# Performance work log

Hardware: AMD Instinct MI355X
Metric: run time of the kernel (lower is better)

Reference implementation:

```python
import jax, jax.numpy as jnp
import numpy as np

L = 28          # num_hidden_layers (kv_cache leading dim = 2*L = 56)
H = 1024        # hidden_size
NH = 8          # num_attention_heads
KVH = 4         # num_key_value_heads
HD = 128        # head_dim
I = 3072        # mlp intermediate size
VC = 4096       # codec vocab size
NCG = 16        # num_code_groups
B = 4
S = 512         # cached seq len
THETA = 1000000.0
EPS = 1e-6


def rmsnorm(x, w):
    v = jnp.mean(jnp.square(x.astype(jnp.float32)), axis=-1, keepdims=True)
    return (x * jax.lax.rsqrt(v + EPS)).astype(x.dtype) * w


def rotate_half(x):
    h = x.shape[-1] // 2
    return jnp.concatenate([-x[..., h:], x[..., :h]], axis=-1)


def setup_inputs() -> dict:
    key = jax.random.key(0)
    ks = jax.random.split(key, 16)
    def f(k, shp, s=0.02):
        return jax.random.normal(k, shp, jnp.float32) * s
    return {
        "cb0_id": jax.random.randint(ks[0], (B, 1), 0, VC),
        "cb1_15_ids": jax.random.randint(ks[1], (B, NCG - 1), 0, VC),
        "trailing_text_embed": f(ks[2], (B, 1, H), 1.0),
        "kv_cache": f(ks[3], (2 * L, B, KVH, S, HD), 1.0),
        "position": jnp.full((B,), S, dtype=jnp.int32),
        "cb0_emb": f(ks[4], (VC, H), 1.0),
        "cp_emb": f(ks[5], (NCG - 1, VC, H), 1.0),
        "Wq": f(ks[6], (L, H, NH * HD)),
        "Wk": f(ks[7], (L, H, KVH * HD)),
        "Wv": f(ks[8], (L, H, KVH * HD)),
        "Wo": f(ks[9], (L, NH * HD, H)),
        "q_norm_w": jnp.ones((L, HD), jnp.float32),
        "k_norm_w": jnp.ones((L, HD), jnp.float32),
        "ln1_w": jnp.ones((L, H), jnp.float32),
        "ln2_w": jnp.ones((L, H), jnp.float32),
        "Wgate": f(ks[10], (L, H, I)),
        "Wup": f(ks[11], (L, H, I)),
        "Wdown": f(ks[12], (L, I, H)),
        "norm_w": jnp.ones((H,), jnp.float32),
        "head_w": f(ks[13], (H, VC)),
    }


def reference(cb0_id, cb1_15_ids, trailing_text_embed, kv_cache, position,
              cb0_emb, cp_emb, Wq, Wk, Wv, Wo, q_norm_w, k_norm_w,
              ln1_w, ln2_w, Wgate, Wup, Wdown, norm_w, head_w):
    n_rep = NH // KVH
    scale = 1.0 / np.sqrt(HD).astype(np.float32)

    # --- codebook embedding sum ---
    e = cb0_emb[cb0_id[:, 0]]                                   # [B,H]
    cp = cp_emb[jnp.arange(NCG - 1)[None, :], cb1_15_ids]       # [B,15,H]
    h = (e + cp.sum(axis=1))[:, None, :] + trailing_text_embed  # [B,1,H]

    # --- rotary at current position; broadcast shape [B,1,1,HD] ---
    inv_freq = 1.0 / (THETA ** (jnp.arange(0, HD, 2, dtype=jnp.float32) / HD))
    freqs = position.astype(jnp.float32)[:, None] * inv_freq[None, :]  # [B,HD/2]
    emb = jnp.concatenate([freqs, freqs], axis=-1)              # [B,HD]
    cos = jnp.cos(emb)[:, None, None, :]
    sin = jnp.sin(emb)[:, None, None, :]

    kv = kv_cache.reshape(L, 2, B, KVH, S, HD)

    def layer(hs, xs):
        wq, wk, wv, wo, qn, kn, l1, l2, wg, wu, wd, kc, vc = xs
        x = rmsnorm(hs, l1)
        q = (x @ wq).reshape(B, 1, NH, HD)
        k = (x @ wk).reshape(B, 1, KVH, HD)
        v = (x @ wv).reshape(B, 1, KVH, HD)
        q = jnp.transpose(rmsnorm(q, qn), (0, 2, 1, 3))   # [B,NH,1,HD]
        k = jnp.transpose(rmsnorm(k, kn), (0, 2, 1, 3))   # [B,KVH,1,HD]
        v = jnp.transpose(v, (0, 2, 1, 3))
        q = q * cos + rotate_half(q) * sin
        k = k * cos + rotate_half(k) * sin
        fk = jnp.concatenate([kc, k], axis=2)             # [B,KVH,S+1,HD]
        fv = jnp.concatenate([vc, v], axis=2)
        # GQA: head h attends kv head h // n_rep == reshape grouping (q_len = 1)
        qg = q.reshape(B, KVH, n_rep, HD)
        scores = jnp.einsum('bgrd,bgsd->bgrs', qg, fk) * scale
        w = jax.nn.softmax(scores.astype(jnp.float32), axis=-1).astype(q.dtype)
        o = jnp.einsum('bgrs,bgsd->bgrd', w, fv).reshape(B, 1, NH * HD)
        hs = hs + o @ wo
        x = rmsnorm(hs, l2)
        hs = hs + (jax.nn.silu(x @ wg) * (x @ wu)) @ wd
        return hs, (k, v)

    xs = (Wq, Wk, Wv, Wo, q_norm_w, k_norm_w, ln1_w, ln2_w,
          Wgate, Wup, Wdown, kv[:, 0], kv[:, 1])
    h, (new_k, new_v) = jax.lax.scan(layer, h, xs)

    h = rmsnorm(h, norm_w)
    past_hidden = h                                       # [B,1,H]
    logits = (h @ head_w)[:, 0, :]                        # [B,VC]

    full_k = jnp.concatenate([kv[:, 0], new_k], axis=3)   # [L,B,KVH,S+1,HD]
    full_v = jnp.concatenate([kv[:, 1], new_v], axis=3)
    new_kv_cache = jnp.stack([full_k, full_v], axis=1).reshape(2 * L, B, KVH, S + 1, HD)
    return logits, new_kv_cache, past_hidden
```

## Files before the change

kernel.cpp:

```cpp
#include <hip/hip_runtime.h>
#include <math.h>

#define L_  28
#define H_  1024
#define NH_ 8
#define KVH_ 4
#define HD_ 128
#define I_  3072
#define VC_ 4096
#define B_  4
#define S_  512
#define EPS_ 1e-6f

#define WS_HA   0
#define WS_HB   4096
#define WS_X1   8192
#define WS_X2   12288
#define WS_XF   16384
#define WS_QKVP 20480
#define WS_ATTO 282624
#define WS_ATML 348160
#define WS_OPP  349184
#define WS_GUP  480256
#define WS_DWP  1266688
#define WS_HDP  1463296

__device__ __forceinline__ float wave_reduce_sum(float v) {
    #pragma unroll
    for (int off = 32; off; off >>= 1) v += __shfl_down(v, off);
    return v;
}
__device__ __forceinline__ float wave_reduce_max(float v) {
    #pragma unroll
    for (int off = 32; off; off >>= 1) v = fmaxf(v, __shfl_down(v, off));
    return v;
}

__global__ __launch_bounds__(256) void k_embed(
    const int* __restrict__ cb0, const int* __restrict__ cb1,
    const float* __restrict__ trail, const float* __restrict__ cb0e,
    const float* __restrict__ cpe, float* __restrict__ hA)
{
    int idx = blockIdx.x * 256 + threadIdx.x;
    int b = idx >> 10, i = idx & 1023;
    float v = cb0e[(size_t)cb0[b] * 1024 + i] + trail[idx];
    #pragma unroll
    for (int j = 0; j < 15; j++)
        v += cpe[((size_t)j * 4096 + cb1[b * 15 + j]) * 1024 + i];
    hA[idx] = v;
}

template<int P>
__global__ __launch_bounds__(1024) void k_norm(
    const float* __restrict__ base, const float* __restrict__ part,
    const float* __restrict__ w, float* __restrict__ hnew,
    float* __restrict__ xout, float* __restrict__ xout2)
{
    __shared__ float red[16];
    const int b = blockIdx.x, k = threadIdx.x;
    float v = base[b * 1024 + k];
    #pragma unroll
    for (int c = 0; c < P; c++) v += part[((size_t)c * 4 + b) * 1024 + k];
    hnew[b * 1024 + k] = v;
    float ss = wave_reduce_sum(v * v);
    if ((k & 63) == 0) red[k >> 6] = ss;
    __syncthreads();
    float tot = 0.f;
    #pragma unroll
    for (int i = 0; i < 16; i++) tot += red[i];
    const float rms = rsqrtf(tot * (1.f / 1024.f) + EPS_);
    const float x = v * rms * w[k];
    xout[b * 1024 + k] = x;
    if (xout2) xout2[b * 1024 + k] = x;
}

template<int RPC, int NTOT>
__device__ __forceinline__ void gemv_tail(
    const float* __restrict__ W, int ldw, int wcol0, int k0,
    const float* __restrict__ xsl, float4* __restrict__ accbuf,
    float* __restrict__ pp, int colblk, int ks)
{
    const int t = threadIdx.x;
    const int wv = t >> 6, lane = t & 63;
    constexpr int RPW = RPC / 4;
    const float4* xs4 = (const float4*)xsl;
    float4 a0 = {0,0,0,0}, a1 = {0,0,0,0}, a2 = {0,0,0,0}, a3 = {0,0,0,0};
    const float* Wp = W + (size_t)(k0 + wv * RPW) * ldw + wcol0 + lane * 4;
    #pragma unroll 8
    for (int i = 0; i < RPW; i++) {
        float4 wvv = *(const float4*)(Wp + (size_t)i * ldw);
        float4 xb = xs4[wv * RPW + i];
        a0.x += wvv.x * xb.x; a0.y += wvv.y * xb.x; a0.z += wvv.z * xb.x; a0.w += wvv.w * xb.x;
        a1.x += wvv.x * xb.y; a1.y += wvv.y * xb.y; a1.z += wvv.z * xb.y; a1.w += wvv.w * xb.y;
        a2.x += wvv.x * xb.z; a2.y += wvv.y * xb.z; a2.z += wvv.z * xb.z; a2.w += wvv.w * xb.z;
        a3.x += wvv.x * xb.w; a3.y += wvv.y * xb.w; a3.z += wvv.z * xb.w; a3.w += wvv.w * xb.w;
    }
    accbuf[(wv * 64 + lane) * 4 + 0] = a0;
    accbuf[(wv * 64 + lane) * 4 + 1] = a1;
    accbuf[(wv * 64 + lane) * 4 + 2] = a2;
    accbuf[(wv * 64 + lane) * 4 + 3] = a3;
    __syncthreads();
    const int l2 = t >> 2, b2 = t & 3;
    float4 s0 = accbuf[(0 * 64 + l2) * 4 + b2];
    float4 s1 = accbuf[(1 * 64 + l2) * 4 + b2];
    float4 s2 = accbuf[(2 * 64 + l2) * 4 + b2];
    float4 s3 = accbuf[(3 * 64 + l2) * 4 + b2];
    float4 s;
    s.x = s0.x + s1.x + s2.x + s3.x;
    s.y = s0.y + s1.y + s2.y + s3.y;
    s.z = s0.z + s1.z + s2.z + s3.z;
    s.w = s0.w + s1.w + s2.w + s3.w;
    *(float4*)(pp + ((size_t)ks * 4 + b2) * NTOT + colblk * 256 + l2 * 4) = s;
}

__global__ __launch_bounds__(256) void k_qkv(
    const float* __restrict__ x1,
    const float* __restrict__ Wq, const float* __restrict__ Wk,
    const float* __restrict__ Wv, float* __restrict__ qkvp)
{
    __shared__ float xsl[128];
    __shared__ float4 accbuf[1024];
    const int t = threadIdx.x;
    const int ks = blockIdx.y, k0 = ks * 32, cb = blockIdx.x;
    if (t < 128) { int kk = t & 31, b = t >> 5; xsl[kk * 4 + b] = x1[b * 1024 + k0 + kk]; }
    __syncthreads();
    const float* W; int ldw, wcol0;
    if (cb < 4)      { W = Wq; ldw = 1024; wcol0 = cb * 256; }
    else if (cb < 6) { W = Wk; ldw = 512;  wcol0 = (cb - 4) * 256; }
    else             { W = Wv; ldw = 512;  wcol0 = (cb - 6) * 256; }
    gemv_tail<32, 2048>(W, ldw, wcol0, k0, xsl, accbuf, qkvp, cb, ks);
}

__global__ __launch_bounds__(256) void k_attn(
    const float* __restrict__ qkvp,
    const float* __restrict__ qnw, const float* __restrict__ knw,
    const float* __restrict__ kin, const float* __restrict__ vin,
    float* __restrict__ kout, float* __restrict__ vout,
    const int* __restrict__ pos,
    float* __restrict__ opart, float* __restrict__ mlpart)
{
    __shared__ float Kl[33][129];
    __shared__ float Vl[33][129];
    __shared__ float ql[2][128];
    __shared__ float sc[2][36];
    __shared__ float red[8];

    const int t = threadIdx.x;
    const int bg = blockIdx.x, b = bg >> 2, g = bg & 3;
    const int c = blockIdx.y;
    const int lane = t & 63;
    const int r = t >> 7, d = t & 127;
    const float scale = 0.088388347648318447f;

    const float posf = (float)pos[b];
    const int j = d & 63;
    const float invf = powf(1.0e6f, -(float)j * (1.0f / 64.0f));
    const float ang = posf * invf;
    const float cs = cosf(ang), sn = sinf(ang);
    const int pd = (d < 64) ? d + 64 : d - 64;

    float qraw = 0.f;
    {
        const int n = (2 * g + r) * 128 + d;
        #pragma unroll
        for (int cc = 0; cc < 32; cc++) qraw += qkvp[((size_t)cc * 4 + b) * 2048 + n];
    }
    ql[r][d] = qraw;
    float ssq = wave_reduce_sum(qraw * qraw);
    if (lane == 0) red[t >> 6] = ssq;
    __syncthreads();
    const float rms_q = rsqrtf((red[r * 2] + red[r * 2 + 1]) * (1.f / 128.f) + EPS_);
    float qv = qraw * rms_q * qnw[d];
    float qp = ql[r][pd] * rms_q * qnw[pd];
    float qro = qv * cs + ((d < 64) ? -qp : qp) * sn;

    float kvraw = 0.f;
    if (c == 15) {
        const int base = (t < 128) ? (1024 + g * 128 + d) : (1536 + g * 128 + d);
        #pragma unroll
        for (int cc = 0; cc < 32; cc++) kvraw += qkvp[((size_t)cc * 4 + b) * 2048 + base];
    }
    float kss = wave_reduce_sum((t < 128) ? kvraw * kvraw : 0.f);
    __syncthreads();
    ql[r][d] = qro;
    if (lane == 0 && t < 128) red[t >> 6] = kss;
    if (c == 15) { if (t < 128) Kl[32][d] = kvraw; else Vl[32][d] = kvraw; }
    __syncthreads();
    float newkv = 0.f;
    if (c == 15) {
        if (t < 128) {
            const float rms_k = rsqrtf((red[0] + red[1]) * (1.f / 128.f) + EPS_);
            float kv_ = Kl[32][d] * rms_k * knw[d];
            float kp  = Kl[32][pd] * rms_k * knw[pd];
            newkv = kv_ * cs + ((d < 64) ? -kp : kp) * sn;
        } else {
            newkv = Vl[32][d];
        }
    }
    __syncthreads();
    const size_t out_bg = (size_t)bg * (513 * 128);
    if (c == 15) {
        if (t < 128) { Kl[32][d] = newkv; kout[out_bg + 512 * 128 + d] = newkv; }
        else         { Vl[32][d] = newkv; vout[out_bg + 512 * 128 + d] = newkv; }
    }

    const size_t in_bg = (size_t)bg * (512 * 128);
    const int s0 = c * 32;
    #pragma unroll
    for (int i = 0; i < 4; i++) {
        int f4 = i * 256 + t;
        int row = f4 >> 5, d0 = (f4 & 31) * 4;
        float4 k4 = *(const float4*)(kin + in_bg + (size_t)(s0 + row) * 128 + d0);
        float4 v4 = *(const float4*)(vin + in_bg + (size_t)(s0 + row) * 128 + d0);
        Kl[row][d0] = k4.x; Kl[row][d0 + 1] = k4.y; Kl[row][d0 + 2] = k4.z; Kl[row][d0 + 3] = k4.w;
        Vl[row][d0] = v4.x; Vl[row][d0 + 1] = v4.y; Vl[row][d0 + 2] = v4.z; Vl[row][d0 + 3] = v4.w;
        *(float4*)(kout + out_bg + (size_t)(s0 + row) * 128 + d0) = k4;
        *(float4*)(vout + out_bg + (size_t)(s0 + row) * 128 + d0) = v4;
    }
    __syncthreads();

    const int nk = (c == 15) ? 33 : 32;
    const int si = d;
    float sv = -1e30f;
    if (si < nk) {
        float a = 0.f;
        #pragma unroll 8
        for (int dd = 0; dd < 128; dd++) a += ql[r][dd] * Kl[si][dd];
        sv = a * scale;
    }
    float mv = wave_reduce_max(sv);
    if (lane == 0) red[t >> 6] = mv;
    __syncthreads();
    const float m = fmaxf(red[r * 2], red[r * 2 + 1]);
    float p = (si < nk) ? expf(sv - m) : 0.f;
    if (si < nk) sc[r][si] = p;
    float lsum = wave_reduce_sum(p);
    __syncthreads();
    if (lane == 0) red[t >> 6] = lsum;
    __syncthreads();
    const float lr = red[r * 2] + red[r * 2 + 1];
    if (d == 0) {
        mlpart[(size_t)((bg * 2 + r) * 16 + c) * 2 + 0] = m;
        mlpart[(size_t)((bg * 2 + r) * 16 + c) * 2 + 1] = lr;
    }
    float o = 0.f;
    for (int s2 = 0; s2 < nk; s2++) o += sc[r][s2] * Vl[s2][d];
    opart[(size_t)((bg * 2 + r) * 16 + c) * 128 + d] = o;
}

__global__ __launch_bounds__(256) void k_oproj(
    const float* __restrict__ atto, const float* __restrict__ atml,
    const float* __restrict__ Wo_l, float* __restrict__ opp)
{
    __shared__ float xsl[128];
    __shared__ float4 accbuf[1024];
    const int t = threadIdx.x;
    const int ks = blockIdx.y, k0 = ks * 32;
    if (t < 128) {
        const int kk = t & 31, b = t >> 5;
        const int nrow = k0 + kk;
        const int head = nrow >> 7, dh = nrow & 127;
        const int g = head >> 1, rr = head & 1;
        const size_t base = (size_t)((b * 4 + g) * 2 + rr) * 16;
        float mc[16], lc[16], M = -1e30f;
        #pragma unroll
        for (int cc = 0; cc < 16; cc++) {
            mc[cc] = atml[(base + cc) * 2];
            lc[cc] = atml[(base + cc) * 2 + 1];
            M = fmaxf(M, mc[cc]);
        }
        float Ls = 0.f, o = 0.f;
        #pragma unroll
        for (int cc = 0; cc < 16; cc++) {
            float wch = expf(mc[cc] - M);
            Ls += lc[cc] * wch;
            o += atto[(base + cc) * 128 + dh] * wch;
        }
        xsl[kk * 4 + b] = o / Ls;
    }
    __syncthreads();
    gemv_tail<32, 1024>(Wo_l, 1024, blockIdx.x * 256, k0, xsl, accbuf, opp, blockIdx.x, ks);
}

__global__ __launch_bounds__(256) void k_gateup(
    const float* __restrict__ x2,
    const float* __restrict__ Wg_l, const float* __restrict__ Wu_l,
    float* __restrict__ gup)
{
    __shared__ float xsl[128];
    __shared__ float4 accbuf[1024];
    const int t = threadIdx.x;
    const int ks = blockIdx.y, k0 = ks * 32, cb = blockIdx.x;
    if (t < 128) { int kk = t & 31, b = t >> 5; xsl[kk * 4 + b] = x2[b * 1024 + k0 + kk]; }
    __syncthreads();
    const float* W; int wcol0;
    if (cb < 12) { W = Wg_l; wcol0 = cb * 256; }
    else         { W = Wu_l; wcol0 = (cb - 12) * 256; }
    gemv_tail<32, 6144>(W, 3072, wcol0, k0, xsl, accbuf, gup, cb, ks);
}

__global__ __launch_bounds__(256) void k_down(
    const float* __restrict__ gup, const float* __restrict__ Wd_l,
    float* __restrict__ dwp)
{
    __shared__ float xsl[256];
    __shared__ float4 accbuf[1024];
    const int t = threadIdx.x;
    const int ks = blockIdx.y, k0 = ks * 64;
    {
        const int b = t >> 6, kk = t & 63;
        float gg = 0.f, uu = 0.f;
        #pragma unroll
        for (int cc = 0; cc < 32; cc++) {
            gg += gup[((size_t)cc * 4 + b) * 6144 + k0 + kk];
            uu += gup[((size_t)cc * 4 + b) * 6144 + 3072 + k0 + kk];
        }
        xsl[kk * 4 + b] = gg / (1.f + expf(-gg)) * uu;
    }
    __syncthreads();
    gemv_tail<64, 1024>(Wd_l, 1024, blockIdx.x * 256, k0, xsl, accbuf, dwp, blockIdx.x, ks);
}

__global__ __launch_bounds__(256) void k_head(
    const float* __restrict__ xf, const float* __restrict__ headw,
    float* __restrict__ hdp)
{
    __shared__ float xsl[128];
    __shared__ float4 accbuf[1024];
    const int t = threadIdx.x;
    const int ks = blockIdx.y, k0 = ks * 32, cb = blockIdx.x;
    if (t < 128) { int kk = t & 31, b = t >> 5; xsl[kk * 4 + b] = xf[b * 1024 + k0 + kk]; }
    __syncthreads();
    gemv_tail<32, 4096>(headw, 4096, cb * 256, k0, xsl, accbuf, hdp, cb, ks);
}

__global__ __launch_bounds__(256) void k_logits(
    const float* __restrict__ hdp, float* __restrict__ logits)
{
    int t4 = blockIdx.x * 256 + threadIdx.x;
    int b = t4 >> 10, n4 = t4 & 1023;
    float4 s = {0.f, 0.f, 0.f, 0.f};
    #pragma unroll
    for (int c = 0; c < 32; c++) {
        float4 v = *(const float4*)(hdp + ((size_t)c * 4 + b) * 4096 + n4 * 4);
        s.x += v.x; s.y += v.y; s.z += v.z; s.w += v.w;
    }
    *(float4*)(logits + (size_t)b * 4096 + n4 * 4) = s;
}

extern "C" void kernel_launch(void* const* d_in, const int* in_sizes, int n_in,
                              void* d_out, int out_size, void* d_ws, size_t ws_size,
                              hipStream_t stream)
{
    const int*   cb0   = (const int*)d_in[0];
    const int*   cb1   = (const int*)d_in[1];
    const float* trail = (const float*)d_in[2];
    const float* kvin  = (const float*)d_in[3];
    const int*   pos   = (const int*)d_in[4];
    const float* cb0e  = (const float*)d_in[5];
    const float* cpe   = (const float*)d_in[6];
    const float* Wq    = (const float*)d_in[7];
    const float* Wk    = (const float*)d_in[8];
    const float* Wv    = (const float*)d_in[9];
    const float* Wo    = (const float*)d_in[10];
    const float* qnw   = (const float*)d_in[11];
    const float* knw   = (const float*)d_in[12];
    const float* ln1   = (const float*)d_in[13];
    const float* ln2   = (const float*)d_in[14];
    const float* Wg    = (const float*)d_in[15];
    const float* Wu    = (const float*)d_in[16];
    const float* Wd    = (const float*)d_in[17];
    const float* normw = (const float*)d_in[18];
    const float* headw = (const float*)d_in[19];

    float* out    = (float*)d_out;
    float* logits = out;
    float* kvout  = out + 16384;
    float* past   = out + 16384 + (size_t)2 * L_ * B_ * KVH_ * (S_ + 1) * HD_;
    float* ws = (float*)d_ws;

    float* hA   = ws + WS_HA;
    float* hB   = ws + WS_HB;
    float* x1   = ws + WS_X1;
    float* x2   = ws + WS_X2;
    float* xf   = ws + WS_XF;
    float* qkvp = ws + WS_QKVP;
    float* atto = ws + WS_ATTO;
    float* atml = ws + WS_ATML;
    float* opp  = ws + WS_OPP;
    float* gup  = ws + WS_GUP;
    float* dwp  = ws + WS_DWP;
    float* hdp  = ws + WS_HDP;

    const size_t IN_PLANE  = (size_t)B_ * KVH_ * S_ * HD_;
    const size_t OUT_PLANE = (size_t)B_ * KVH_ * (S_ + 1) * HD_;

    k_embed<<<16, 256, 0, stream>>>(cb0, cb1, trail, cb0e, cpe, hA);

    for (int l = 0; l < L_; l++) {
        if (l == 0)
            k_norm<0><<<4, 1024, 0, stream>>>(hA, dwp, ln1 + (size_t)l * H_, hB, x1, nullptr);
        else
            k_norm<48><<<4, 1024, 0, stream>>>(hA, dwp, ln1 + (size_t)l * H_, hB, x1, nullptr);
        k_qkv<<<dim3(8, 32), 256, 0, stream>>>(
            x1, Wq + (size_t)l * H_ * 1024, Wk + (size_t)l * H_ * 512,
            Wv + (size_t)l * H_ * 512, qkvp);
        k_attn<<<dim3(16, 16), 256, 0, stream>>>(
            qkvp, qnw + (size_t)l * HD_, knw + (size_t)l * HD_,
            kvin + (size_t)(2 * l) * IN_PLANE, kvin + (size_t)(2 * l + 1) * IN_PLANE,
            kvout + (size_t)(2 * l) * OUT_PLANE, kvout + (size_t)(2 * l + 1) * OUT_PLANE,
            pos, atto, atml);
        k_oproj<<<dim3(4, 32), 256, 0, stream>>>(
            atto, atml, Wo + (size_t)l * 1024 * H_, opp);
        k_norm<32><<<4, 1024, 0, stream>>>(hB, opp, ln2 + (size_t)l * H_, hA, x2, nullptr);
        k_gateup<<<dim3(24, 32), 256, 0, stream>>>(
            x2, Wg + (size_t)l * H_ * I_, Wu + (size_t)l * H_ * I_, gup);
        k_down<<<dim3(4, 48), 256, 0, stream>>>(
            gup, Wd + (size_t)l * I_ * H_, dwp);
    }
    k_norm<48><<<4, 1024, 0, stream>>>(hA, dwp, normw, hB, xf, past);
    k_head<<<dim3(16, 32), 256, 0, stream>>>(xf, headw, hdp);
    k_logits<<<16, 256, 0, stream>>>(hdp, logits);
}
```

Measured before the change: 1.190 ms.

## Fuse RMSNorm into GEMVs and replace split-K partial buffers with atomic accumulation

Removes the separate norm and logits-reduction kernels. Each GEMV block now recomputes the RMS statistics of the residual and normalizes its own input slice, and split-K results are accumulated directly into the residual and output buffers with float atomics instead of partial arrays reduced later. Buffers that the next stage accumulates into are zeroed inside earlier kernels, and weights are prefetched into registers before the prologue so loads overlap the norm work. This cuts launches and partial-buffer traffic per layer, at the cost of redundant norm reductions in every block and nondeterministic atomic summation order.

```diff
diff --git a/kernel.cpp b/kernel.cpp
--- a/kernel.cpp
+++ b/kernel.cpp
@@ -12,18 +12,11 @@
 #define S_  512
 #define EPS_ 1e-6f
 
-#define WS_HA   0
-#define WS_HB   4096
-#define WS_X1   8192
-#define WS_X2   12288
-#define WS_XF   16384
-#define WS_QKVP 20480
-#define WS_ATTO 282624
-#define WS_ATML 348160
-#define WS_OPP  349184
-#define WS_GUP  480256
-#define WS_DWP  1266688
-#define WS_HDP  1463296
+#define WS_H    0
+#define WS_QKVB 4096
+#define WS_ATTO 12288
+#define WS_ATML 77824
+#define WS_GUPB 78848
 
 __device__ __forceinline__ float wave_reduce_sum(float v) {
     #pragma unroll
@@ -34,12 +27,27 @@
     #pragma unroll
     for (int off = 32; off; off >>= 1) v = fmaxf(v, __shfl_down(v, off));
     return v;
+}
+
+__device__ __forceinline__ void reduce4(float ss[4], float* red, int t) {
+    int lane = t & 63, wv = t >> 6;
+    #pragma unroll
+    for (int b = 0; b < 4; b++) {
+        float v = wave_reduce_sum(ss[b]);
+        if (lane == 0) red[b * 4 + wv] = v;
+    }
+    __syncthreads();
+    #pragma unroll
+    for (int b = 0; b < 4; b++)
+        ss[b] = red[b * 4] + red[b * 4 + 1] + red[b * 4 + 2] + red[b * 4 + 3];
+    __syncthreads();
 }
 
 __global__ __launch_bounds__(256) void k_embed(
     const int* __restrict__ cb0, const int* __restrict__ cb1,
     const float* __restrict__ trail, const float* __restrict__ cb0e,
-    const float* __restrict__ cpe, float* __restrict__ hA)
+    const float* __restrict__ cpe, float* __restrict__ hcur,
+    float* __restrict__ qkvb, float* __restrict__ logits)
 {
     int idx = blockIdx.x * 256 + threadIdx.x;
     int b = idx >> 10, i = idx & 1023;
@@ -47,53 +55,35 @@
     #pragma unroll
     for (int j = 0; j < 15; j++)
         v += cpe[((size_t)j * 4096 + cb1[b * 15 + j]) * 1024 + i];
-    hA[idx] = v;
-}
-
-template<int P>
-__global__ __launch_bounds__(1024) void k_norm(
-    const float* __restrict__ base, const float* __restrict__ part,
-    const float* __restrict__ w, float* __restrict__ hnew,
-    float* __restrict__ xout, float* __restrict__ xout2)
-{
-    __shared__ float red[16];
-    const int b = blockIdx.x, k = threadIdx.x;
-    float v = base[b * 1024 + k];
-    #pragma unroll
-    for (int c = 0; c < P; c++) v += part[((size_t)c * 4 + b) * 1024 + k];
-    hnew[b * 1024 + k] = v;
-    float ss = wave_reduce_sum(v * v);
-    if ((k & 63) == 0) red[k >> 6] = ss;
-    __syncthreads();
-    float tot = 0.f;
-    #pragma unroll
-    for (int i = 0; i < 16; i++) tot += red[i];
-    const float rms = rsqrtf(tot * (1.f / 1024.f) + EPS_);
-    const float x = v * rms * w[k];
-    xout[b * 1024 + k] = x;
-    if (xout2) xout2[b * 1024 + k] = x;
-}
-
-template<int RPC, int NTOT>
-__device__ __forceinline__ void gemv_tail(
+    hcur[idx] = v;
+    float4 z = {0.f, 0.f, 0.f, 0.f};
+    *(float4*)(logits + (size_t)idx * 4) = z;
+    qkvb[idx * 2] = 0.f; qkvb[idx * 2 + 1] = 0.f;
+}
+
+template<int RPW, typename F>
+__device__ __forceinline__ void gemv_atomic(
     const float* __restrict__ W, int ldw, int wcol0, int k0,
     const float* __restrict__ xsl, float4* __restrict__ accbuf,
-    float* __restrict__ pp, int colblk, int ks)
+    float* __restrict__ outp, int outstride, int outcol0, F&& prologue)
 {
     const int t = threadIdx.x;
     const int wv = t >> 6, lane = t & 63;
-    constexpr int RPW = RPC / 4;
+    const float* Wp = W + (size_t)(k0 + wv * RPW) * ldw + wcol0 + lane * 4;
+    float4 wreg[RPW];
+    #pragma unroll
+    for (int i = 0; i < RPW; i++) wreg[i] = *(const float4*)(Wp + (size_t)i * ldw);
+    prologue();
     const float4* xs4 = (const float4*)xsl;
     float4 a0 = {0,0,0,0}, a1 = {0,0,0,0}, a2 = {0,0,0,0}, a3 = {0,0,0,0};
-    const float* Wp = W + (size_t)(k0 + wv * RPW) * ldw + wcol0 + lane * 4;
-    #pragma unroll 8
+    #pragma unroll
     for (int i = 0; i < RPW; i++) {
-        float4 wvv = *(const float4*)(Wp + (size_t)i * ldw);
+        float4 w4 = wreg[i];
         float4 xb = xs4[wv * RPW + i];
-        a0.x += wvv.x * xb.x; a0.y += wvv.y * xb.x; a0.z += wvv.z * xb.x; a0.w += wvv.w * xb.x;
-        a1.x += wvv.x * xb.y; a1.y += wvv.y * xb.y; a1.z += wvv.z * xb.y; a1.w += wvv.w * xb.y;
-        a2.x += wvv.x * xb.z; a2.y += wvv.y * xb.z; a2.z += wvv.z * xb.z; a2.w += wvv.w * xb.z;
-        a3.x += wvv.x * xb.w; a3.y += wvv.y * xb.w; a3.z += wvv.z * xb.w; a3.w += wvv.w * xb.w;
+        a0.x += w4.x * xb.x; a0.y += w4.y * xb.x; a0.z += w4.z * xb.x; a0.w += w4.w * xb.x;
+        a1.x += w4.x * xb.y; a1.y += w4.y * xb.y; a1.z += w4.z * xb.y; a1.w += w4.w * xb.y;
+        a2.x += w4.x * xb.z; a2.y += w4.y * xb.z; a2.z += w4.z * xb.z; a2.w += w4.w * xb.z;
+        a3.x += w4.x * xb.w; a3.y += w4.y * xb.w; a3.z += w4.z * xb.w; a3.w += w4.w * xb.w;
     }
     accbuf[(wv * 64 + lane) * 4 + 0] = a0;
     accbuf[(wv * 64 + lane) * 4 + 1] = a1;
@@ -101,38 +91,49 @@
     accbuf[(wv * 64 + lane) * 4 + 3] = a3;
     __syncthreads();
     const int l2 = t >> 2, b2 = t & 3;
-    float4 s0 = accbuf[(0 * 64 + l2) * 4 + b2];
-    float4 s1 = accbuf[(1 * 64 + l2) * 4 + b2];
-    float4 s2 = accbuf[(2 * 64 + l2) * 4 + b2];
-    float4 s3 = accbuf[(3 * 64 + l2) * 4 + b2];
-    float4 s;
-    s.x = s0.x + s1.x + s2.x + s3.x;
-    s.y = s0.y + s1.y + s2.y + s3.y;
-    s.z = s0.z + s1.z + s2.z + s3.z;
-    s.w = s0.w + s1.w + s2.w + s3.w;
-    *(float4*)(pp + ((size_t)ks * 4 + b2) * NTOT + colblk * 256 + l2 * 4) = s;
+    float4 s = {0,0,0,0};
+    #pragma unroll
+    for (int w = 0; w < 4; w++) {
+        float4 sv = accbuf[(w * 64 + l2) * 4 + b2];
+        s.x += sv.x; s.y += sv.y; s.z += sv.z; s.w += sv.w;
+    }
+    float* op = outp + (size_t)b2 * outstride + outcol0 + l2 * 4;
+    unsafeAtomicAdd(op + 0, s.x);
+    unsafeAtomicAdd(op + 1, s.y);
+    unsafeAtomicAdd(op + 2, s.z);
+    unsafeAtomicAdd(op + 3, s.w);
 }
 
 __global__ __launch_bounds__(256) void k_qkv(
-    const float* __restrict__ x1,
+    const float* __restrict__ hcur, const float* __restrict__ ln1,
     const float* __restrict__ Wq, const float* __restrict__ Wk,
-    const float* __restrict__ Wv, float* __restrict__ qkvp)
+    const float* __restrict__ Wv, float* __restrict__ qkvb)
 {
     __shared__ float xsl[128];
     __shared__ float4 accbuf[1024];
+    __shared__ float red[16];
     const int t = threadIdx.x;
     const int ks = blockIdx.y, k0 = ks * 32, cb = blockIdx.x;
-    if (t < 128) { int kk = t & 31, b = t >> 5; xsl[kk * 4 + b] = x1[b * 1024 + k0 + kk]; }
-    __syncthreads();
-    const float* W; int ldw, wcol0;
-    if (cb < 4)      { W = Wq; ldw = 1024; wcol0 = cb * 256; }
-    else if (cb < 6) { W = Wk; ldw = 512;  wcol0 = (cb - 4) * 256; }
-    else             { W = Wv; ldw = 512;  wcol0 = (cb - 6) * 256; }
-    gemv_tail<32, 2048>(W, ldw, wcol0, k0, xsl, accbuf, qkvp, cb, ks);
+    const float* W; int ldw, wcol0, ocol0;
+    if (cb < 4)      { W = Wq; ldw = 1024; wcol0 = cb * 256;      ocol0 = cb * 256; }
+    else if (cb < 6) { W = Wk; ldw = 512;  wcol0 = (cb - 4) * 256; ocol0 = 1024 + (cb - 4) * 256; }
+    else             { W = Wv; ldw = 512;  wcol0 = (cb - 6) * 256; ocol0 = 1536 + (cb - 6) * 256; }
+    gemv_atomic<8>(W, ldw, wcol0, k0, xsl, accbuf, qkvb, 2048, ocol0, [&]() {
+        float ss[4] = {0, 0, 0, 0};
+        #pragma unroll
+        for (int i = 0; i < 16; i++) { float v = hcur[t + 256 * i]; ss[i >> 2] += v * v; }
+        reduce4(ss, red, t);
+        if (t < 128) {
+            int kk = t & 31, b = t >> 5;
+            float rms = rsqrtf(ss[b] * (1.f / 1024.f) + EPS_);
+            xsl[kk * 4 + b] = hcur[b * 1024 + k0 + kk] * rms * ln1[k0 + kk];
+        }
+        __syncthreads();
+    });
 }
 
 __global__ __launch_bounds__(256) void k_attn(
-    const float* __restrict__ qkvp,
+    const float* __restrict__ qkvb,
     const float* __restrict__ qnw, const float* __restrict__ knw,
     const float* __restrict__ kin, const float* __restrict__ vin,
     float* __restrict__ kout, float* __restrict__ vout,
@@ -154,17 +155,12 @@
 
     const float posf = (float)pos[b];
     const int j = d & 63;
-    const float invf = powf(1.0e6f, -(float)j * (1.0f / 64.0f));
+    const float invf = exp2f(-(float)j * 0.31143075889569021f);
     const float ang = posf * invf;
     const float cs = cosf(ang), sn = sinf(ang);
     const int pd = (d < 64) ? d + 64 : d - 64;
 
-    float qraw = 0.f;
-    {
-        const int n = (2 * g + r) * 128 + d;
-        #pragma unroll
-        for (int cc = 0; cc < 32; cc++) qraw += qkvp[((size_t)cc * 4 + b) * 2048 + n];
-    }
+    float qraw = qkvb[b * 2048 + (2 * g + r) * 128 + d];
     ql[r][d] = qraw;
     float ssq = wave_reduce_sum(qraw * qraw);
     if (lane == 0) red[t >> 6] = ssq;
@@ -176,9 +172,9 @@
 
     float kvraw = 0.f;
     if (c == 15) {
-        const int base = (t < 128) ? (1024 + g * 128 + d) : (1536 + g * 128 + d);
-        #pragma unroll
-        for (int cc = 0; cc < 32; cc++) kvraw += qkvp[((size_t)cc * 4 + b) * 2048 + base];
+        const int base = (t < 128) ? (b * 2048 + 1024 + g * 128 + d)
+                                   : (b * 2048 + 1536 + g * 128 + d);
+        kvraw = qkvb[base];
     }
     float kss = wave_reduce_sum((t < 128) ? kvraw * kvraw : 0.f);
     __syncthreads();
@@ -250,102 +246,114 @@
 
 __global__ __launch_bounds__(256) void k_oproj(
     const float* __restrict__ atto, const float* __restrict__ atml,
-    const float* __restrict__ Wo_l, float* __restrict__ opp)
+    const float* __restrict__ Wo_l, float* __restrict__ hcur,
+    float* __restrict__ gupb)
 {
     __shared__ float xsl[128];
     __shared__ float4 accbuf[1024];
     const int t = threadIdx.x;
-    const int ks = blockIdx.y, k0 = ks * 32;
-    if (t < 128) {
-        const int kk = t & 31, b = t >> 5;
-        const int nrow = k0 + kk;
-        const int head = nrow >> 7, dh = nrow & 127;
-        const int g = head >> 1, rr = head & 1;
-        const size_t base = (size_t)((b * 4 + g) * 2 + rr) * 16;
-        float mc[16], lc[16], M = -1e30f;
-        #pragma unroll
-        for (int cc = 0; cc < 16; cc++) {
-            mc[cc] = atml[(base + cc) * 2];
-            lc[cc] = atml[(base + cc) * 2 + 1];
-            M = fmaxf(M, mc[cc]);
-        }
-        float Ls = 0.f, o = 0.f;
-        #pragma unroll
-        for (int cc = 0; cc < 16; cc++) {
-            float wch = expf(mc[cc] - M);
-            Ls += lc[cc] * wch;
-            o += atto[(base + cc) * 128 + dh] * wch;
-        }
-        xsl[kk * 4 + b] = o / Ls;
-    }
-    __syncthreads();
-    gemv_tail<32, 1024>(Wo_l, 1024, blockIdx.x * 256, k0, xsl, accbuf, opp, blockIdx.x, ks);
+    const int ks = blockIdx.y, k0 = ks * 32, cb = blockIdx.x;
+    gemv_atomic<8>(Wo_l, 1024, cb * 256, k0, xsl, accbuf, hcur, 1024, cb * 256, [&]() {
+        const int bl = ks * 4 + cb;
+        if (t < 192) gupb[bl * 192 + t] = 0.f;
+        if (t < 128) {
+            const int kk = t & 31, b = t >> 5;
+            const int nrow = k0 + kk;
+            const int head = nrow >> 7, dh = nrow & 127;
+            const int g = head >> 1, rr = head & 1;
+            const size_t base = (size_t)((b * 4 + g) * 2 + rr) * 16;
+            float mc[16], lc[16], M = -1e30f;
+            #pragma unroll
+            for (int cc = 0; cc < 16; cc++) {
+                mc[cc] = atml[(base + cc) * 2];
+                lc[cc] = atml[(base + cc) * 2 + 1];
+                M = fmaxf(M, mc[cc]);
+            }
+            float Ls = 0.f, o = 0.f;
+            #pragma unroll
+            for (int cc = 0; cc < 16; cc++) {
+                float wch = expf(mc[cc] - M);
+                Ls += lc[cc] * wch;
+                o += atto[(base + cc) * 128 + dh] * wch;
+            }
+            xsl[kk * 4 + b] = o / Ls;
+        }
+        __syncthreads();
+    });
 }
 
 __global__ __launch_bounds__(256) void k_gateup(
-    const float* __restrict__ x2,
+    const float* __restrict__ hcur, const float* __restrict__ ln2,
     const float* __restrict__ Wg_l, const float* __restrict__ Wu_l,
-    float* __restrict__ gup)
+    float* __restrict__ gupb)
 {
     __shared__ float xsl[128];
     __shared__ float4 accbuf[1024];
+    __shared__ float red[16];
     const int t = threadIdx.x;
     const int ks = blockIdx.y, k0 = ks * 32, cb = blockIdx.x;
-    if (t < 128) { int kk = t & 31, b = t >> 5; xsl[kk * 4 + b] = x2[b * 1024 + k0 + kk]; }
-    __syncthreads();
-    const float* W; int wcol0;
-    if (cb < 12) { W = Wg_l; wcol0 = cb * 256; }
-    else         { W = Wu_l; wcol0 = (cb - 12) * 256; }
-    gemv_tail<32, 6144>(W, 3072, wcol0, k0, xsl, accbuf, gup, cb, ks);
+    const float* W; int wcol0, ocol0;
+    if (cb < 12) { W = Wg_l; wcol0 = cb * 256;        ocol0 = cb * 256; }
+    else         { W = Wu_l; wcol0 = (cb - 12) * 256; ocol0 = 3072 + (cb - 12) * 256; }
+    gemv_atomic<8>(W, 3072, wcol0, k0, xsl, accbuf, gupb, 6144, ocol0, [&]() {
+        float ss[4] = {0, 0, 0, 0};
+        #pragma unroll
+        for (int i = 0; i < 16; i++) { float v = hcur[t + 256 * i]; ss[i >> 2] += v * v; }
+        reduce4(ss, red, t);
+        if (t < 128) {
+            int kk = t & 31, b = t >> 5;
+            float rms = rsqrtf(ss[b] * (1.f / 1024.f) + EPS_);
+            xsl[kk * 4 + b] = hcur[b * 1024 + k0 + kk] * rms * ln2[k0 + kk];
+        }
+        __syncthreads();
+    });
 }
 
 __global__ __launch_bounds__(256) void k_down(
-    const float* __restrict__ gup, const float* __restrict__ Wd_l,
-    float* __restrict__ dwp)
-{
-    __shared__ float xsl[256];
-    __shared__ float4 accbuf[1024];
-    const int t = threadIdx.x;
-    const int ks = blockIdx.y, k0 = ks * 64;
-    {
-        const int b = t >> 6, kk = t & 63;
-        float gg = 0.f, uu = 0.f;
-        #pragma unroll
-        for (int cc = 0; cc < 32; cc++) {
-            gg += gup[((size_t)cc * 4 + b) * 6144 + k0 + kk];
-            uu += gup[((size_t)cc * 4 + b) * 6144 + 3072 + k0 + kk];
-        }
-        xsl[kk * 4 + b] = gg / (1.f + expf(-gg)) * uu;
-    }
-    __syncthreads();
-    gemv_tail<64, 1024>(Wd_l, 1024, blockIdx.x * 256, k0, xsl, accbuf, dwp, blockIdx.x, ks);
-}
-
-__global__ __launch_bounds__(256) void k_head(
-    const float* __restrict__ xf, const float* __restrict__ headw,
-    float* __restrict__ hdp)
+    const float* __restrict__ gupb, const float* __restrict__ Wd_l,
+    float* __restrict__ hcur, float* __restrict__ qkvb)
 {
     __shared__ float xsl[128];
     __shared__ float4 accbuf[1024];
     const int t = threadIdx.x;
     const int ks = blockIdx.y, k0 = ks * 32, cb = blockIdx.x;
-    if (t < 128) { int kk = t & 31, b = t >> 5; xsl[kk * 4 + b] = xf[b * 1024 + k0 + kk]; }
-    __syncthreads();
-    gemv_tail<32, 4096>(headw, 4096, cb * 256, k0, xsl, accbuf, hdp, cb, ks);
-}
-
-__global__ __launch_bounds__(256) void k_logits(
-    const float* __restrict__ hdp, float* __restrict__ logits)
-{
-    int t4 = blockIdx.x * 256 + threadIdx.x;
-    int b = t4 >> 10, n4 = t4 & 1023;
-    float4 s = {0.f, 0.f, 0.f, 0.f};
-    #pragma unroll
-    for (int c = 0; c < 32; c++) {
-        float4 v = *(const float4*)(hdp + ((size_t)c * 4 + b) * 4096 + n4 * 4);
-        s.x += v.x; s.y += v.y; s.z += v.z; s.w += v.w;
-    }
-    *(float4*)(logits + (size_t)b * 4096 + n4 * 4) = s;
+    gemv_atomic<8>(Wd_l, 1024, cb * 256, k0, xsl, accbuf, hcur, 1024, cb * 256, [&]() {
+        const int bl = ks * 4 + cb;
+        if (bl < 128 && t < 64) qkvb[bl * 64 + t] = 0.f;
+        if (t < 128) {
+            int kk = t & 31, b = t >> 5;
+            float gg = gupb[b * 6144 + k0 + kk];
+            float uu = gupb[b * 6144 + 3072 + k0 + kk];
+            xsl[kk * 4 + b] = gg / (1.f + expf(-gg)) * uu;
+        }
+        __syncthreads();
+    });
+}
+
+__global__ __launch_bounds__(256) void k_head(
+    const float* __restrict__ hcur, const float* __restrict__ normw,
+    const float* __restrict__ headw, float* __restrict__ logits,
+    float* __restrict__ past)
+{
+    __shared__ float xsl[128];
+    __shared__ float4 accbuf[1024];
+    __shared__ float red[16];
+    const int t = threadIdx.x;
+    const int ks = blockIdx.y, k0 = ks * 32, cb = blockIdx.x;
+    gemv_atomic<8>(headw, 4096, cb * 256, k0, xsl, accbuf, logits, 4096, cb * 256, [&]() {
+        float ss[4] = {0, 0, 0, 0};
+        #pragma unroll
+        for (int i = 0; i < 16; i++) { float v = hcur[t + 256 * i]; ss[i >> 2] += v * v; }
+        reduce4(ss, red, t);
+        if (t < 128) {
+            int kk = t & 31, b = t >> 5;
+            float rms = rsqrtf(ss[b] * (1.f / 1024.f) + EPS_);
+            float x = hcur[b * 1024 + k0 + kk] * rms * normw[k0 + kk];
+            xsl[kk * 4 + b] = x;
+            if (cb == 0) past[b * 1024 + k0 + kk] = x;
+        }
+        __syncthreads();
+    });
 }
 
 extern "C" void kernel_launch(void* const* d_in, const int* in_sizes, int n_in,
@@ -379,46 +387,34 @@
     float* past   = out + 16384 + (size_t)2 * L_ * B_ * KVH_ * (S_ + 1) * HD_;
     float* ws = (float*)d_ws;
 
-    float* hA   = ws + WS_HA;
-    float* hB   = ws + WS_HB;
-    float* x1   = ws + WS_X1;
-    float* x2   = ws + WS_X2;
-    float* xf   = ws + WS_XF;
-    float* qkvp = ws + WS_QKVP;
+    float* hcur = ws + WS_H;
+    float* qkvb = ws + WS_QKVB;
     float* atto = ws + WS_ATTO;
     float* atml = ws + WS_ATML;
-    float* opp  = ws + WS_OPP;
-    float* gup  = ws + WS_GUP;
-    float* dwp  = ws + WS_DWP;
-    float* hdp  = ws + WS_HDP;
+    float* gupb = ws + WS_GUPB;
 
     const size_t IN_PLANE  = (size_t)B_ * KVH_ * S_ * HD_;
     const size_t OUT_PLANE = (size_t)B_ * KVH_ * (S_ + 1) * HD_;
 
-    k_embed<<<16, 256, 0, stream>>>(cb0, cb1, trail, cb0e, cpe, hA);
+    k_embed<<<16, 256, 0, stream>>>(cb0, cb1, trail, cb0e, cpe, hcur, qkvb, logits);
 
     for (int l = 0; l < L_; l++) {
-        if (l == 0)
-            k_norm<0><<<4, 1024, 0, stream>>>(hA, dwp, ln1 + (size_t)l * H_, hB, x1, nullptr);
-        else
-            k_norm<48><<<4, 1024, 0, stream>>>(hA, dwp, ln1 + (size_t)l * H_, hB, x1, nullptr);
         k_qkv<<<dim3(8, 32), 256, 0, stream>>>(
-            x1, Wq + (size_t)l * H_ * 1024, Wk + (size_t)l * H_ * 512,
-            Wv + (size_t)l * H_ * 512, qkvp);
+            hcur, ln1 + (size_t)l * H_,
+            Wq + (size_t)l * H_ * 1024, Wk + (size_t)l * H_ * 512,
+            Wv + (size_t)l * H_ * 512, qkvb);
         k_attn<<<dim3(16, 16), 256, 0, stream>>>(
-            qkvp, qnw + (size_t)l * HD_, knw + (size_t)l * HD_,
+            qkvb, qnw + (size_t)l * HD_, knw + (size_t)l * HD_,
             kvin + (size_t)(2 * l) * IN_PLANE, kvin + (size_t)(2 * l + 1) * IN_PLANE,
             kvout + (size_t)(2 * l) * OUT_PLANE, kvout + (size_t)(2 * l + 1) * OUT_PLANE,
             pos, atto, atml);
         k_oproj<<<dim3(4, 32), 256, 0, stream>>>(
-            atto, atml, Wo + (size_t)l * 1024 * H_, opp);
-        k_norm<32><<<4, 1024, 0, stream>>>(hB, opp, ln2 + (size_t)l * H_, hA, x2, nullptr);
+            atto, atml, Wo + (size_t)l * 1024 * H_, hcur, gupb);
         k_gateup<<<dim3(24, 32), 256, 0, stream>>>(
-            x2, Wg + (size_t)l * H_ * I_, Wu + (size_t)l * H_ * I_, gup);
-        k_down<<<dim3(4, 48), 256, 0, stream>>>(
-            gup, Wd + (size_t)l * I_ * H_, dwp);
-    }
-    k_norm<48><<<4, 1024, 0, stream>>>(hA, dwp, normw, hB, xf, past);
-    k_head<<<dim3(16, 32), 256, 0, stream>>>(xf, headw, hdp);
-    k_logits<<<16, 256, 0, stream>>>(hdp, logits);
-}
+            hcur, ln2 + (size_t)l * H_,
+            Wg + (size_t)l * H_ * I_, Wu + (size_t)l * H_ * I_, gupb);
+        k_down<<<dim3(4, 96), 256, 0, stream>>>(
+            gupb, Wd + (size_t)l * I_ * H_, hcur, qkvb);
+    }
+    k_head<<<dim3(16, 32), 256, 0, stream>>>(hcur, normw, headw, logits, past);
+}
```

Result: slower. 1.554 ms (+30.5%).

## Fuse RMSNorm and split-K reduction into GEMV kernels via last-block atomic fold

Applied to the files above, without the earlier changes.

Removes the standalone k_norm and k_logits launches. Each split-K GEMV kernel now uses an atomic counter so the last four blocks per column group sum the partials, add the residual into h, and write per-chunk sums of squares. The next GEMV applies RMSNorm on the fly from those partial sums. This cuts 57 kernel launches and the serial single-block norm kernels, at the cost of atomics, threadfences and a serialized tail in the final blocks. The RoPE frequency pow is also replaced by exp2f.

```diff
diff --git a/kernel.cpp b/kernel.cpp
--- a/kernel.cpp
+++ b/kernel.cpp
@@ -12,18 +12,17 @@
 #define S_  512
 #define EPS_ 1e-6f
 
-#define WS_HA   0
-#define WS_HB   4096
-#define WS_X1   8192
-#define WS_X2   12288
-#define WS_XF   16384
-#define WS_QKVP 20480
-#define WS_ATTO 282624
-#define WS_ATML 348160
-#define WS_OPP  349184
-#define WS_GUP  480256
-#define WS_DWP  1266688
-#define WS_HDP  1463296
+#define WS_H     0
+#define WS_SSQ1P 4096
+#define WS_SSQ2P 4160
+#define WS_CNT   4224
+#define WS_QKVP  4256
+#define WS_ATTO  266400
+#define WS_ATML  331936
+#define WS_OPP   333984
+#define WS_GUP   465056
+#define WS_DWP   1251488
+#define WS_HDP   1448096
 
 __device__ __forceinline__ float wave_reduce_sum(float v) {
     #pragma unroll
@@ -39,39 +38,20 @@
 __global__ __launch_bounds__(256) void k_embed(
     const int* __restrict__ cb0, const int* __restrict__ cb1,
     const float* __restrict__ trail, const float* __restrict__ cb0e,
-    const float* __restrict__ cpe, float* __restrict__ hA)
-{
-    int idx = blockIdx.x * 256 + threadIdx.x;
-    int b = idx >> 10, i = idx & 1023;
-    float v = cb0e[(size_t)cb0[b] * 1024 + i] + trail[idx];
+    const float* __restrict__ cpe, float* __restrict__ h,
+    float* __restrict__ ssq1p, int* __restrict__ cnt)
+{
+    const int x = blockIdx.x, t = threadIdx.x;
+    const int b = x >> 2, q = x & 3;
+    const int i = q * 256 + t;
+    float v = cb0e[(size_t)cb0[b] * 1024 + i] + trail[b * 1024 + i];
     #pragma unroll
     for (int j = 0; j < 15; j++)
         v += cpe[((size_t)j * 4096 + cb1[b * 15 + j]) * 1024 + i];
-    hA[idx] = v;
-}
-
-template<int P>
-__global__ __launch_bounds__(1024) void k_norm(
-    const float* __restrict__ base, const float* __restrict__ part,
-    const float* __restrict__ w, float* __restrict__ hnew,
-    float* __restrict__ xout, float* __restrict__ xout2)
-{
-    __shared__ float red[16];
-    const int b = blockIdx.x, k = threadIdx.x;
-    float v = base[b * 1024 + k];
-    #pragma unroll
-    for (int c = 0; c < P; c++) v += part[((size_t)c * 4 + b) * 1024 + k];
-    hnew[b * 1024 + k] = v;
-    float ss = wave_reduce_sum(v * v);
-    if ((k & 63) == 0) red[k >> 6] = ss;
-    __syncthreads();
-    float tot = 0.f;
-    #pragma unroll
-    for (int i = 0; i < 16; i++) tot += red[i];
-    const float rms = rsqrtf(tot * (1.f / 1024.f) + EPS_);
-    const float x = v * rms * w[k];
-    xout[b * 1024 + k] = x;
-    if (xout2) xout2[b * 1024 + k] = x;
+    h[b * 1024 + i] = v;
+    float s = wave_reduce_sum(v * v);
+    if ((t & 63) == 0) ssq1p[(q * 4 + (t >> 6)) * 4 + b] = s;
+    if (x == 0 && t < 24) cnt[t] = 0;
 }
 
 template<int RPC, int NTOT>
@@ -113,8 +93,45 @@
     *(float4*)(pp + ((size_t)ks * 4 + b2) * NTOT + colblk * 256 + l2 * 4) = s;
 }
 
+template<int NCH, bool ADD_H>
+__device__ __forceinline__ void split_fold(
+    const float* __restrict__ part, float* __restrict__ hbuf,
+    float* __restrict__ outbuf, int NT,
+    float* __restrict__ ssqp, int* __restrict__ cntp, int cb)
+{
+    __shared__ int oldsh;
+    __shared__ float tmp[16];
+    const int t = threadIdx.x;
+    __syncthreads();
+    if (t == 0) {
+        __threadfence();
+        oldsh = atomicAdd(cntp, 1);
+        __threadfence();
+    }
+    __syncthreads();
+    const int old = oldsh;
+    if (old < NCH - 4) return;
+    const int sub = old - (NCH - 4);
+    const int col = cb * 256 + sub * 64 + (t >> 2);
+    const int b = t & 3;
+    float acc = ADD_H ? hbuf[b * 1024 + col] : 0.f;
+    #pragma unroll 8
+    for (int c = 0; c < NCH; c++) acc += part[(size_t)(c * 4 + b) * NT + col];
+    outbuf[(size_t)b * NT + col] = acc;
+    if (ssqp) {
+        float v = acc * acc;
+        #pragma unroll
+        for (int off = 32; off >= 4; off >>= 1) v += __shfl_down(v, off);
+        if ((t & 63) < 4) tmp[(t >> 6) * 4 + (t & 3)] = v;
+        __syncthreads();
+        if (t < 4) ssqp[(cb * 4 + sub) * 4 + t] = tmp[t] + tmp[4 + t] + tmp[8 + t] + tmp[12 + t];
+    }
+    if (old == NCH - 1 && t == 0) *cntp = 0;
+}
+
 __global__ __launch_bounds__(256) void k_qkv(
-    const float* __restrict__ x1,
+    const float* __restrict__ h, const float* __restrict__ ssq1p,
+    const float* __restrict__ ln1,
     const float* __restrict__ Wq, const float* __restrict__ Wk,
     const float* __restrict__ Wv, float* __restrict__ qkvp)
 {
@@ -122,7 +139,14 @@
     __shared__ float4 accbuf[1024];
     const int t = threadIdx.x;
     const int ks = blockIdx.y, k0 = ks * 32, cb = blockIdx.x;
-    if (t < 128) { int kk = t & 31, b = t >> 5; xsl[kk * 4 + b] = x1[b * 1024 + k0 + kk]; }
+    if (t < 128) {
+        const int kk = t & 31, b = t >> 5;
+        float ssq = 0.f;
+        #pragma unroll
+        for (int i = 0; i < 16; i++) ssq += ssq1p[i * 4 + b];
+        const float rms = rsqrtf(ssq * (1.f / 1024.f) + EPS_);
+        xsl[kk * 4 + b] = h[b * 1024 + k0 + kk] * rms * ln1[k0 + kk];
+    }
     __syncthreads();
     const float* W; int ldw, wcol0;
     if (cb < 4)      { W = Wq; ldw = 1024; wcol0 = cb * 256; }
@@ -154,7 +178,7 @@
 
     const float posf = (float)pos[b];
     const int j = d & 63;
-    const float invf = powf(1.0e6f, -(float)j * (1.0f / 64.0f));
+    const float invf = exp2f(-(float)j * 0.31143075889569021f);
     const float ang = posf * invf;
     const float cs = cosf(ang), sn = sinf(ang);
     const int pd = (d < 64) ? d + 64 : d - 64;
@@ -250,12 +274,13 @@
 
 __global__ __launch_bounds__(256) void k_oproj(
     const float* __restrict__ atto, const float* __restrict__ atml,
-    const float* __restrict__ Wo_l, float* __restrict__ opp)
+    const float* __restrict__ Wo_l, float* __restrict__ opp,
+    float* __restrict__ h, float* __restrict__ ssq2p, int* __restrict__ cnt)
 {
     __shared__ float xsl[128];
     __shared__ float4 accbuf[1024];
     const int t = threadIdx.x;
-    const int ks = blockIdx.y, k0 = ks * 32;
+    const int ks = blockIdx.y, k0 = ks * 32, cb = blockIdx.x;
     if (t < 128) {
         const int kk = t & 31, b = t >> 5;
         const int nrow = k0 + kk;
@@ -279,11 +304,13 @@
         xsl[kk * 4 + b] = o / Ls;
     }
     __syncthreads();
-    gemv_tail<32, 1024>(Wo_l, 1024, blockIdx.x * 256, k0, xsl, accbuf, opp, blockIdx.x, ks);
+    gemv_tail<32, 1024>(Wo_l, 1024, cb * 256, k0, xsl, accbuf, opp, cb, ks);
+    split_fold<32, true>(opp, h, h, 1024, ssq2p, &cnt[cb], cb);
 }
 
 __global__ __launch_bounds__(256) void k_gateup(
-    const float* __restrict__ x2,
+    const float* __restrict__ h, const float* __restrict__ ssq2p,
+    const float* __restrict__ ln2,
     const float* __restrict__ Wg_l, const float* __restrict__ Wu_l,
     float* __restrict__ gup)
 {
@@ -291,7 +318,14 @@
     __shared__ float4 accbuf[1024];
     const int t = threadIdx.x;
     const int ks = blockIdx.y, k0 = ks * 32, cb = blockIdx.x;
-    if (t < 128) { int kk = t & 31, b = t >> 5; xsl[kk * 4 + b] = x2[b * 1024 + k0 + kk]; }
+    if (t < 128) {
+        const int kk = t & 31, b = t >> 5;
+        float ssq = 0.f;
+        #pragma unroll
+        for (int i = 0; i < 16; i++) ssq += ssq2p[i * 4 + b];
+        const float rms = rsqrtf(ssq * (1.f / 1024.f) + EPS_);
+        xsl[kk * 4 + b] = h[b * 1024 + k0 + kk] * rms * ln2[k0 + kk];
+    }
     __syncthreads();
     const float* W; int wcol0;
     if (cb < 12) { W = Wg_l; wcol0 = cb * 256; }
@@ -301,12 +335,13 @@
 
 __global__ __launch_bounds__(256) void k_down(
     const float* __restrict__ gup, const float* __restrict__ Wd_l,
-    float* __restrict__ dwp)
+    float* __restrict__ dwp, float* __restrict__ h,
+    float* __restrict__ ssq1p, int* __restrict__ cnt)
 {
     __shared__ float xsl[256];
     __shared__ float4 accbuf[1024];
     const int t = threadIdx.x;
-    const int ks = blockIdx.y, k0 = ks * 64;
+    const int ks = blockIdx.y, k0 = ks * 64, cb = blockIdx.x;
     {
         const int b = t >> 6, kk = t & 63;
         float gg = 0.f, uu = 0.f;
@@ -318,34 +353,33 @@
         xsl[kk * 4 + b] = gg / (1.f + expf(-gg)) * uu;
     }
     __syncthreads();
-    gemv_tail<64, 1024>(Wd_l, 1024, blockIdx.x * 256, k0, xsl, accbuf, dwp, blockIdx.x, ks);
+    gemv_tail<64, 1024>(Wd_l, 1024, cb * 256, k0, xsl, accbuf, dwp, cb, ks);
+    split_fold<48, true>(dwp, h, h, 1024, ssq1p, &cnt[4 + cb], cb);
 }
 
 __global__ __launch_bounds__(256) void k_head(
-    const float* __restrict__ xf, const float* __restrict__ headw,
-    float* __restrict__ hdp)
+    const float* __restrict__ h, const float* __restrict__ ssq1p,
+    const float* __restrict__ normw, const float* __restrict__ headw,
+    float* __restrict__ hdp, float* __restrict__ logits,
+    float* __restrict__ past, int* __restrict__ cnt)
 {
     __shared__ float xsl[128];
     __shared__ float4 accbuf[1024];
     const int t = threadIdx.x;
     const int ks = blockIdx.y, k0 = ks * 32, cb = blockIdx.x;
-    if (t < 128) { int kk = t & 31, b = t >> 5; xsl[kk * 4 + b] = xf[b * 1024 + k0 + kk]; }
+    if (t < 128) {
+        const int kk = t & 31, b = t >> 5;
+        float ssq = 0.f;
+        #pragma unroll
+        for (int i = 0; i < 16; i++) ssq += ssq1p[i * 4 + b];
+        const float rms = rsqrtf(ssq * (1.f / 1024.f) + EPS_);
+        float x = h[b * 1024 + k0 + kk] * rms * normw[k0 + kk];
+        xsl[kk * 4 + b] = x;
+        if (cb == 0) past[b * 1024 + k0 + kk] = x;
+    }
     __syncthreads();
     gemv_tail<32, 4096>(headw, 4096, cb * 256, k0, xsl, accbuf, hdp, cb, ks);
-}
-
-__global__ __launch_bounds__(256) void k_logits(
-    const float* __restrict__ hdp, float* __restrict__ logits)
-{
-    int t4 = blockIdx.x * 256 + threadIdx.x;
-    int b = t4 >> 10, n4 = t4 & 1023;
-    float4 s = {0.f, 0.f, 0.f, 0.f};
-    #pragma unroll
-    for (int c = 0; c < 32; c++) {
-        float4 v = *(const float4*)(hdp + ((size_t)c * 4 + b) * 4096 + n4 * 4);
-        s.x += v.x; s.y += v.y; s.z += v.z; s.w += v.w;
-    }
-    *(float4*)(logits + (size_t)b * 4096 + n4 * 4) = s;
+    split_fold<32, false>(hdp, nullptr, logits, 4096, nullptr, &cnt[8 + cb], cb);
 }
 
 extern "C" void kernel_launch(void* const* d_in, const int* in_sizes, int n_in,
@@ -379,31 +413,27 @@
     float* past   = out + 16384 + (size_t)2 * L_ * B_ * KVH_ * (S_ + 1) * HD_;
     float* ws = (float*)d_ws;
 
-    float* hA   = ws + WS_HA;
-    float* hB   = ws + WS_HB;
-    float* x1   = ws + WS_X1;
-    float* x2   = ws + WS_X2;
-    float* xf   = ws + WS_XF;
-    float* qkvp = ws + WS_QKVP;
-    float* atto = ws + WS_ATTO;
-    float* atml = ws + WS_ATML;
-    float* opp  = ws + WS_OPP;
-    float* gup  = ws + WS_GUP;
-    float* dwp  = ws + WS_DWP;
-    float* hdp  = ws + WS_HDP;
+    float* h     = ws + WS_H;
+    float* ssq1p = ws + WS_SSQ1P;
+    float* ssq2p = ws + WS_SSQ2P;
+    int*   cnt   = (int*)(ws + WS_CNT);
+    float* qkvp  = ws + WS_QKVP;
+    float* atto  = ws + WS_ATTO;
+    float* atml  = ws + WS_ATML;
+    float* opp   = ws + WS_OPP;
+    float* gup   = ws + WS_GUP;
+    float* dwp   = ws + WS_DWP;
+    float* hdp   = ws + WS_HDP;
 
     const size_t IN_PLANE  = (size_t)B_ * KVH_ * S_ * HD_;
     const size_t OUT_PLANE = (size_t)B_ * KVH_ * (S_ + 1) * HD_;
 
-    k_embed<<<16, 256, 0, stream>>>(cb0, cb1, trail, cb0e, cpe, hA);
+    k_embed<<<16, 256, 0, stream>>>(cb0, cb1, trail, cb0e, cpe, h, ssq1p, cnt);
 
     for (int l = 0; l < L_; l++) {
-        if (l == 0)
-            k_norm<0><<<4, 1024, 0, stream>>>(hA, dwp, ln1 + (size_t)l * H_, hB, x1, nullptr);
-        else
-            k_norm<48><<<4, 1024, 0, stream>>>(hA, dwp, ln1 + (size_t)l * H_, hB, x1, nullptr);
         k_qkv<<<dim3(8, 32), 256, 0, stream>>>(
-            x1, Wq + (size_t)l * H_ * 1024, Wk + (size_t)l * H_ * 512,
+            h, ssq1p, ln1 + (size_t)l * H_,
+            Wq + (size_t)l * H_ * 1024, Wk + (size_t)l * H_ * 512,
             Wv + (size_t)l * H_ * 512, qkvp);
         k_attn<<<dim3(16, 16), 256, 0, stream>>>(
             qkvp, qnw + (size_t)l * HD_, knw + (size_t)l * HD_,
@@ -411,14 +441,12 @@
             kvout + (size_t)(2 * l) * OUT_PLANE, kvout + (size_t)(2 * l + 1) * OUT_PLANE,
             pos, atto, atml);
         k_oproj<<<dim3(4, 32), 256, 0, stream>>>(
-            atto, atml, Wo + (size_t)l * 1024 * H_, opp);
-        k_norm<32><<<4, 1024, 0, stream>>>(hB, opp, ln2 + (size_t)l * H_, hA, x2, nullptr);
+            atto, atml, Wo + (size_t)l * 1024 * H_, opp, h, ssq2p, cnt);
         k_gateup<<<dim3(24, 32), 256, 0, stream>>>(
-            x2, Wg + (size_t)l * H_ * I_, Wu + (size_t)l * H_ * I_, gup);
+            h, ssq2p, ln2 + (size_t)l * H_,
+            Wg + (size_t)l * H_ * I_, Wu + (size_t)l * H_ * I_, gup);
         k_down<<<dim3(4, 48), 256, 0, stream>>>(
-            gup, Wd + (size_t)l * I_ * H_, dwp);
-    }
-    k_norm<48><<<4, 1024, 0, stream>>>(hA, dwp, normw, hB, xf, past);
-    k_head<<<dim3(16, 32), 256, 0, stream>>>(xf, headw, hdp);
-    k_logits<<<16, 256, 0, stream>>>(hdp, logits);
-}
+            gup, Wd + (size_t)l * I_ * H_, dwp, h, ssq1p, cnt);
+    }
+    k_head<<<dim3(16, 32), 256, 0, stream>>>(h, ssq1p, normw, headw, hdp, logits, past, cnt);
+}
```

Result: slower. 1.520 ms (+27.7%).
